# Kernel optimization log

Measured on AMD Instinct MI355X. Metric: run time of the kernel, lower is better.

The kernel has to match this reference:

```python
import jax, jax.numpy as jnp
import numpy as np

N_NODES = 300000   # cell instances
N_NETS  = 200000   # hyperedges (nets); each net has exactly one source/driver
E_SINK  = 1000000  # sink (node->net) pin edges
NODE_DIM, NET_DIM, EMB = 32, 16, 64
L, NUM_VN = 3, 1000
OUT_NODE, OUT_NET = 4, 4
SLOPE = 0.01  # torch leaky_relu default negative_slope


def leaky(x):
    return jnp.where(x >= 0, x, SLOPE * x)


def _lin(key, fan_in, fan_out):
    kw, kb = jax.random.split(key)
    b = 1.0 / np.sqrt(fan_in)
    W = jax.random.uniform(kw, (fan_in, fan_out), jnp.float32, -b, b)
    bb = jax.random.uniform(kb, (fan_out,), jnp.float32, -b, b)
    return W, bb


def setup_inputs() -> dict:
    key = jax.random.key(0)
    ks = iter(jax.random.split(key, 64))
    d = {}
    d["node_features"] = jax.random.normal(next(ks), (N_NODES, NODE_DIM), jnp.float32)
    d["net_features"] = jax.random.normal(next(ks), (N_NETS, NET_DIM), jnp.float32)
    d["src_nodes"] = jax.random.randint(next(ks), (N_NETS,), 0, N_NODES)   # driver node of net i
    d["sink_nodes"] = jax.random.randint(next(ks), (E_SINK,), 0, N_NODES)
    d["sink_nets"] = jax.random.randint(next(ks), (E_SINK,), 0, N_NETS)
    d["edge_weight"] = jax.random.uniform(next(ks), (E_SINK,), jnp.float32)
    d["batch"] = jax.random.randint(next(ks), (N_NODES,), 0, NUM_VN)       # node -> virtual node id
    # node / net encoders
    d["ne_W1"], d["ne_b1"] = _lin(next(ks), NODE_DIM, 2 * EMB)
    d["ne_W2"], d["ne_b2"] = _lin(next(ks), 2 * EMB, EMB)
    d["te_W1"], d["te_b1"] = _lin(next(ks), NET_DIM, EMB)
    d["te_W2"], d["te_b2"] = _lin(next(ks), EMB, EMB)
    d["vn_emb"] = jnp.zeros((EMB,), jnp.float32)  # torch: init.constant_(weight, 0)
    # HyperConv layers, stacked over L
    Wnet, bnet, Wnode, bnode = [], [], [], []
    for _ in range(L):
        W, b = _lin(next(ks), 3 * EMB, EMB); Wnet.append(W); bnet.append(b)
        W, b = _lin(next(ks), 2 * EMB, EMB); Wnode.append(W); bnode.append(b)
    d["conv_Wnet"] = jnp.stack(Wnet); d["conv_bnet"] = jnp.stack(bnet)
    d["conv_Wnode"] = jnp.stack(Wnode); d["conv_bnode"] = jnp.stack(bnode)
    # virtual-node MLPs (L-1 of them)
    vW1, vb1, vW2, vb2 = [], [], [], []
    for _ in range(L - 1):
        W, b = _lin(next(ks), EMB, EMB); vW1.append(W); vb1.append(b)
        W, b = _lin(next(ks), EMB, EMB); vW2.append(W); vb2.append(b)
    d["vn_W1"] = jnp.stack(vW1); d["vn_b1"] = jnp.stack(vb1)
    d["vn_W2"] = jnp.stack(vW2); d["vn_b2"] = jnp.stack(vb2)
    # output heads
    d["fc1n_W"], d["fc1n_b"] = _lin(next(ks), EMB, 256)
    d["fc2n_W"], d["fc2n_b"] = _lin(next(ks), 256, OUT_NODE)
    d["fc1e_W"], d["fc1e_b"] = _lin(next(ks), EMB, 64)
    d["fc2e_W"], d["fc2e_b"] = _lin(next(ks), 64, OUT_NET)
    return d


def _forward(node_features, net_features, edge_weight,
             ne_W1, ne_b1, ne_W2, ne_b2, te_W1, te_b1, te_W2, te_b2,
             vn_emb, conv_Wnet, conv_bnet, conv_Wnode, conv_bnode,
             vn_W1, vn_b1, vn_W2, vn_b2,
             fc1n_W, fc1n_b, fc2n_W, fc2n_b, fc1e_W, fc1e_b, fc2e_W, fc2e_b,
             src_nodes, sink_nodes, sink_nets, batch):
    h = leaky(node_features @ ne_W1 + ne_b1) @ ne_W2 + ne_b2   # [N, EMB]
    g = leaky(net_features @ te_W1 + te_b1) @ te_W2 + te_b2    # [M, EMB]
    w = edge_weight[:, None]
    vn = jnp.broadcast_to(vn_emb, (NUM_VN, EMB))               # embedding of all-zero indices
    for l in range(L):
        h = h + vn[batch]
        # node -> net (hyperedge) aggregation: driver message + weighted sink sum
        agg_src = h[src_nodes]                                             # [M, EMB]
        agg_sink = jax.ops.segment_sum(h[sink_nodes] * w, sink_nets, num_segments=N_NETS)
        g = jnp.concatenate([g, agg_src, agg_sink], axis=-1) @ conv_Wnet[l] + conv_bnet[l]
        # net -> node aggregation
        back = jax.ops.segment_sum(g, src_nodes, num_segments=N_NODES) \
             + jax.ops.segment_sum(g[sink_nets] * w, sink_nodes, num_segments=N_NODES)
        h = jnp.concatenate([h, back], axis=-1) @ conv_Wnode[l] + conv_bnode[l]
        h = leaky(h)
        g = leaky(g)
        if l < L - 1:
            pooled = jax.ops.segment_max(h, batch, num_segments=NUM_VN)   # global_max_pool
            tmp = pooled + vn
            vn = vn + (leaky(tmp @ vn_W1[l] + vn_b1[l]) @ vn_W2[l] + vn_b2[l])
    node_rep = jnp.abs(leaky(h @ fc1n_W + fc1n_b) @ fc2n_W + fc2n_b)
    net_rep = jnp.abs(leaky(g @ fc1e_W + fc1e_b) @ fc2e_W + fc2e_b)
    return node_rep, net_rep


def reference(node_features, net_features, edge_weight,
              ne_W1, ne_b1, ne_W2, ne_b2, te_W1, te_b1, te_W2, te_b2,
              vn_emb, conv_Wnet, conv_bnet, conv_Wnode, conv_bnode,
              vn_W1, vn_b1, vn_W2, vn_b2,
              fc1n_W, fc1n_b, fc2n_W, fc2n_b, fc1e_W, fc1e_b, fc2e_W, fc2e_b,
              src_nodes, sink_nodes, sink_nets, batch):
    return _forward(node_features, net_features, edge_weight,
                    ne_W1, ne_b1, ne_W2, ne_b2, te_W1, te_b1, te_W2, te_b2,
                    vn_emb, conv_Wnet, conv_bnet, conv_Wnode, conv_bnode,
                    vn_W1, vn_b1, vn_W2, vn_b2,
                    fc1n_W, fc1n_b, fc2n_W, fc2n_b, fc1e_W, fc1e_b, fc2e_W, fc2e_b,
                    src_nodes, sink_nodes, sink_nets, batch)
```

## Files before the change

### kernel.cpp

```cpp
#include <hip/hip_runtime.h>
#include <cstdint>

static constexpr int N_NODES = 300000;
static constexpr int N_NETS  = 200000;
static constexpr int E_SINK  = 1000000;
static constexpr int NODE_DIM = 32;
static constexpr int NET_DIM  = 16;
static constexpr int EMB = 64;
static constexpr int NUM_VN = 1000;
#define SLOPE 0.01f

typedef __attribute__((ext_vector_type(8))) short bhalf8;
typedef __attribute__((ext_vector_type(4))) float floatx4;

__device__ __forceinline__ float leaky(float x) { return x >= 0.f ? x : SLOPE * x; }

__device__ __forceinline__ unsigned bf16_rne(float x) {
    unsigned u = __float_as_uint(x);
    return (u + 0x7FFFu + ((u >> 16) & 1u)) >> 16;
}
__device__ __forceinline__ void split8(const float* x, bhalf8& ah, bhalf8& al) {
#pragma unroll
    for (int e = 0; e < 8; ++e) {
        unsigned h = bf16_rne(x[e]);
        float fh = __uint_as_float(h << 16);
        unsigned l = bf16_rne(x[e] - fh);
        ah[e] = (short)h; al[e] = (short)l;
    }
}

template<bool LK>
__device__ __forceinline__ void afrag_g(const float* rowp, int kbase, bhalf8& ah, bhalf8& al) {
    float4 v0 = *(const float4*)(rowp + kbase);
    float4 v1 = *(const float4*)(rowp + kbase + 4);
    float x[8] = {v0.x, v0.y, v0.z, v0.w, v1.x, v1.y, v1.z, v1.w};
    if (LK) {
#pragma unroll
        for (int e = 0; e < 8; ++e) x[e] = leaky(x[e]);
    }
    split8(x, ah, al);
}

__device__ __forceinline__ void afrag_l(const float* tp, bhalf8& ah, bhalf8& al) {
    float4 v0 = *(const float4*)tp;
    float4 v1 = *(const float4*)(tp + 4);
    float x[8] = {v0.x, v0.y, v0.z, v0.w, v1.x, v1.y, v1.z, v1.w};
    split8(x, ah, al);
}

__device__ __forceinline__ void wfrag(const float* W, int cols, int K, int col, bool colok,
                                      int kt, int g, bhalf8& wh, bhalf8& wl) {
    float x[8];
#pragma unroll
    for (int e = 0; e < 8; ++e) {
        int k = kt * 32 + g * 8 + e;
        x[e] = (k < K && colok) ? W[(size_t)k * cols + col] : 0.f;
    }
    split8(x, wh, wl);
}

__device__ __forceinline__ floatx4 mm3(bhalf8 ah, bhalf8 al, bhalf8 wh, bhalf8 wl, floatx4 c) {
    c = __builtin_amdgcn_mfma_f32_16x16x32_bf16(ah, wh, c, 0, 0, 0);
    c = __builtin_amdgcn_mfma_f32_16x16x32_bf16(ah, wl, c, 0, 0, 0);
    c = __builtin_amdgcn_mfma_f32_16x16x32_bf16(al, wh, c, 0, 0, 0);
    return c;
}

__global__ void k_hist_edges(const int* __restrict__ sink_nets, const int* __restrict__ sink_nodes,
                             int* __restrict__ cnt_net, int* __restrict__ cnt_node)
{
    int e = blockIdx.x * 256 + threadIdx.x;
    if (e >= E_SINK) return;
    atomicAdd(&cnt_net[sink_nets[e]], 1);
    atomicAdd(&cnt_node[sink_nodes[e]], 1);
}

__global__ void k_hist_misc(const int* __restrict__ src_nodes, const int* __restrict__ batch,
                            int* __restrict__ cnt_src, int* __restrict__ cnt_vn)
{
    int i = blockIdx.x * 256 + threadIdx.x;
    if (i < N_NETS) atomicAdd(&cnt_src[src_nodes[i]], 1);
    if (i < N_NODES) atomicAdd(&cnt_vn[batch[i]], 1);
}

__global__ void k_scan1(const int* __restrict__ cnt, int n, int* __restrict__ bsum) {
    __shared__ int s[256];
    int i = blockIdx.x * 256 + threadIdx.x;
    s[threadIdx.x] = (i < n) ? cnt[i] : 0;
    __syncthreads();
    for (int off = 128; off; off >>= 1) {
        if (threadIdx.x < off) s[threadIdx.x] += s[threadIdx.x + off];
        __syncthreads();
    }
    if (threadIdx.x == 0) bsum[blockIdx.x] = s[0];
}

__global__ void k_scan2(int* __restrict__ data, int n) {
    __shared__ int s[256];
    __shared__ int carry_s;
    int tid = threadIdx.x;
    if (tid == 0) carry_s = 0;
    __syncthreads();
    for (int base = 0; base < n; base += 256) {
        int i = base + tid;
        int v = (i < n) ? data[i] : 0;
        s[tid] = v;
        __syncthreads();
        for (int off = 1; off < 256; off <<= 1) {
            int t = (tid >= off) ? s[tid - off] : 0;
            __syncthreads();
            s[tid] += t;
            __syncthreads();
        }
        int excl = s[tid] - v + carry_s;
        if (i < n) data[i] = excl;
        __syncthreads();
        if (tid == 255) carry_s = excl + v;
        __syncthreads();
    }
}

__global__ void k_scan3(const int* __restrict__ cnt, int n, const int* __restrict__ bsum,
                        int* __restrict__ start) {
    __shared__ int s[256];
    int i = blockIdx.x * 256 + threadIdx.x;
    int v = (i < n) ? cnt[i] : 0;
    s[threadIdx.x] = v;
    __syncthreads();
    for (int off = 1; off < 256; off <<= 1) {
        int t = (threadIdx.x >= off) ? s[threadIdx.x - off] : 0;
        __syncthreads();
        s[threadIdx.x] += t;
        __syncthreads();
    }
    int excl = s[threadIdx.x] - v + bsum[blockIdx.x];
    if (i < n) start[i] = excl;
    if (i == n - 1) start[n] = excl + v;
}

__global__ void k_fill_edges(const int* __restrict__ sink_nets, const int* __restrict__ sink_nodes,
                             const float* __restrict__ ew,
                             const int* __restrict__ net_start, const int* __restrict__ node_start,
                             int* __restrict__ cur_net, int* __restrict__ cur_node,
                             int* __restrict__ e_node, float* __restrict__ e_w,
                             int* __restrict__ e2_net, float* __restrict__ e2_w)
{
    int e = blockIdx.x * 256 + threadIdx.x;
    if (e >= E_SINK) return;
    int tn = sink_nets[e], dn = sink_nodes[e];
    float w = ew[e];
    int p = net_start[tn] + atomicAdd(&cur_net[tn], 1);
    e_node[p] = dn; e_w[p] = w;
    int q = node_start[dn] + atomicAdd(&cur_node[dn], 1);
    e2_net[q] = tn; e2_w[q] = w;
}

__global__ void k_fill_misc(const int* __restrict__ src_nodes, const int* __restrict__ batch,
                            const int* __restrict__ src_start, const int* __restrict__ vn_start,
                            int* __restrict__ cur_src, int* __restrict__ cur_vn,
                            int* __restrict__ s_net, int* __restrict__ b_node)
{
    int i = blockIdx.x * 256 + threadIdx.x;
    if (i < N_NETS) {
        int d = src_nodes[i];
        int p = src_start[d] + atomicAdd(&cur_src[d], 1);
        s_net[p] = i;
    }
    if (i < N_NODES) {
        int v = batch[i];
        int p = vn_start[v] + atomicAdd(&cur_vn[v], 1);
        b_node[p] = i;
    }
}

__global__ __launch_bounds__(256) void k_gather_agg(
    float* __restrict__ agg, const float* __restrict__ h,
    const int* __restrict__ net_start, const int* __restrict__ e_node, const float* __restrict__ e_w)
{
    int w = (blockIdx.x * 256 + threadIdx.x) >> 6;
    if (w >= N_NETS) return;
    int lane = threadIdx.x & 63;
    int grp = lane >> 4, l15 = lane & 15;
    int j0 = net_start[w], j1 = net_start[w + 1];
    float ax = 0.f, ay = 0.f, az = 0.f, aw = 0.f;
    for (int j = j0 + grp; j < j1; j += 4) {
        int idx = e_node[j];
        float wt = e_w[j];
        float4 v = ((const float4*)(h + (size_t)idx * 64))[l15];
        ax += wt * v.x; ay += wt * v.y; az += wt * v.z; aw += wt * v.w;
    }
    ax += __shfl_xor(ax, 16, 64); ay += __shfl_xor(ay, 16, 64);
    az += __shfl_xor(az, 16, 64); aw += __shfl_xor(aw, 16, 64);
    ax += __shfl_xor(ax, 32, 64); ay += __shfl_xor(ay, 32, 64);
    az += __shfl_xor(az, 32, 64); aw += __shfl_xor(aw, 32, 64);
    if (grp == 0)
        ((float4*)(agg + (size_t)w * 64))[l15] = make_float4(ax, ay, az, aw);
}

__global__ __launch_bounds__(256) void k_gather_back(
    float* __restrict__ back, const float* __restrict__ g,
    const int* __restrict__ src_start, const int* __restrict__ s_net,
    const int* __restrict__ node_start, const int* __restrict__ e2_net, const float* __restrict__ e2_w)
{
    int w = (blockIdx.x * 256 + threadIdx.x) >> 6;
    if (w >= N_NODES) return;
    int lane = threadIdx.x & 63;
    int grp = lane >> 4, l15 = lane & 15;
    float ax = 0.f, ay = 0.f, az = 0.f, aw = 0.f;
    int j0 = src_start[w], j1 = src_start[w + 1];
    for (int j = j0 + grp; j < j1; j += 4) {
        int idx = s_net[j];
        float4 v = ((const float4*)(g + (size_t)idx * 64))[l15];
        ax += v.x; ay += v.y; az += v.z; aw += v.w;
    }
    j0 = node_start[w]; j1 = node_start[w + 1];
    for (int j = j0 + grp; j < j1; j += 4) {
        int idx = e2_net[j];
        float wt = e2_w[j];
        float4 v = ((const float4*)(g + (size_t)idx * 64))[l15];
        ax += wt * v.x; ay += wt * v.y; az += wt * v.z; aw += wt * v.w;
    }
    ax += __shfl_xor(ax, 16, 64); ay += __shfl_xor(ay, 16, 64);
    az += __shfl_xor(az, 16, 64); aw += __shfl_xor(aw, 16, 64);
    ax += __shfl_xor(ax, 32, 64); ay += __shfl_xor(ay, 32, 64);
    az += __shfl_xor(az, 32, 64); aw += __shfl_xor(aw, 32, 64);
    if (grp == 0)
        ((float4*)(back + (size_t)w * 64))[l15] = make_float4(ax, ay, az, aw);
}

__global__ __launch_bounds__(256) void k_pool_gather(
    float* __restrict__ pooled, const float* __restrict__ h,
    const int* __restrict__ vn_start, const int* __restrict__ b_node)
{
    __shared__ float4 red[16][16];
    int tid = threadIdx.x;
    int grp = tid >> 4, l15 = tid & 15;
    int v = blockIdx.x;
    int j0 = vn_start[v], j1 = vn_start[v + 1];
    const float NEG = -__builtin_inff();
    float mx = NEG, my = NEG, mz = NEG, mw = NEG;
    for (int j = j0 + grp; j < j1; j += 16) {
        int nd = b_node[j];
        float4 val = ((const float4*)(h + (size_t)nd * 64))[l15];
        mx = fmaxf(mx, val.x); my = fmaxf(my, val.y);
        mz = fmaxf(mz, val.z); mw = fmaxf(mw, val.w);
    }
    red[grp][l15] = make_float4(mx, my, mz, mw);
    __syncthreads();
    if (tid < 16) {
        float4 m = red[0][tid];
#pragma unroll
        for (int q = 1; q < 16; ++q) {
            float4 r = red[q][tid];
            m.x = fmaxf(m.x, r.x); m.y = fmaxf(m.y, r.y);
            m.z = fmaxf(m.z, r.z); m.w = fmaxf(m.w, r.w);
        }
        ((float4*)(pooled + (size_t)v * 64))[tid] = m;
    }
}

__global__ __launch_bounds__(256) void k_node_enc_mfma(
    const float* __restrict__ x, const float* __restrict__ W1, const float* __restrict__ b1,
    const float* __restrict__ W2, const float* __restrict__ b2, float* __restrict__ h)
{
    __shared__ __align__(16) float t[64][132];
    int lane = threadIdx.x & 63, wid = threadIdx.x >> 6;
    int g16 = lane >> 4, l15 = lane & 15;
    int rbase = blockIdx.x * 64;

    bhalf8 W1H[2], W1L[2];
#pragma unroll
    for (int s = 0; s < 2; ++s)
        wfrag(W1, 128, 32, wid * 16 + s * 64 + l15, true, 0, g16, W1H[s], W1L[s]);
    bhalf8 W2H[4], W2L[4];
#pragma unroll
    for (int kt = 0; kt < 4; ++kt)
        wfrag(W2, 64, 128, wid * 16 + l15, true, kt, g16, W2H[kt], W2L[kt]);

#pragma unroll
    for (int ms = 0; ms < 4; ++ms) {
        int r = min(rbase + ms * 16 + l15, N_NODES - 1);
        bhalf8 ah, al;
        afrag_g<false>(x + (size_t)r * NODE_DIM, g16 * 8, ah, al);
#pragma unroll
        for (int s = 0; s < 2; ++s) {
            floatx4 acc = {0.f, 0.f, 0.f, 0.f};
            acc = mm3(ah, al, W1H[s], W1L[s], acc);
            int hc = wid * 16 + s * 64 + l15;
            float bb = b1[hc];
#pragma unroll
            for (int i = 0; i < 4; ++i)
                t[ms * 16 + g16 * 4 + i][hc] = leaky(acc[i] + bb);
        }
    }
    __syncthreads();

    int cs = wid * 16 + l15;
    float bias = b2[cs];
#pragma unroll
    for (int ms = 0; ms < 4; ++ms) {
        floatx4 acc = {0.f, 0.f, 0.f, 0.f};
#pragma unroll
        for (int kt = 0; kt < 4; ++kt) {
            bhalf8 ah, al;
            afrag_l(&t[ms * 16 + l15][kt * 32 + g16 * 8], ah, al);
            acc = mm3(ah, al, W2H[kt], W2L[kt], acc);
        }
#pragma unroll
        for (int i = 0; i < 4; ++i) {
            int r = rbase + ms * 16 + g16 * 4 + i;
            if (r < N_NODES) h[(size_t)r * 64 + cs] = acc[i] + bias;
        }
    }
}

__global__ __launch_bounds__(256) void k_net_enc_mfma(
    const float* __restrict__ x, const float* __restrict__ W1, const float* __restrict__ b1,
    const float* __restrict__ W2, const float* __restrict__ b2, float* __restrict__ g)
{
    __shared__ __align__(16) float t[64][68];
    int lane = threadIdx.x & 63, wid = threadIdx.x >> 6;
    int g16 = lane >> 4, l15 = lane & 15;
    int rbase = blockIdx.x * 64;
    int cs = wid * 16 + l15;

    bhalf8 W1H, W1L;
    wfrag(W1, 64, 16, cs, true, 0, g16, W1H, W1L);
    bhalf8 W2H[2], W2L[2];
#pragma unroll
    for (int kt = 0; kt < 2; ++kt)
        wfrag(W2, 64, 64, cs, true, kt, g16, W2H[kt], W2L[kt]);

#pragma unroll
    for (int ms = 0; ms < 4; ++ms) {
        int r = min(rbase + ms * 16 + l15, N_NETS - 1);
        bhalf8 ah = {0,0,0,0,0,0,0,0}, al = {0,0,0,0,0,0,0,0};
        if (g16 < 2) afrag_g<false>(x + (size_t)r * NET_DIM, g16 * 8, ah, al);
        floatx4 acc = {0.f, 0.f, 0.f, 0.f};
        acc = mm3(ah, al, W1H, W1L, acc);
        float bb = b1[cs];
#pragma unroll
        for (int i = 0; i < 4; ++i)
            t[ms * 16 + g16 * 4 + i][cs] = leaky(acc[i] + bb);
    }
    __syncthreads();

    float bias = b2[cs];
#pragma unroll
    for (int ms = 0; ms < 4; ++ms) {
        floatx4 acc = {0.f, 0.f, 0.f, 0.f};
#pragma unroll
        for (int kt = 0; kt < 2; ++kt) {
            bhalf8 ah, al;
            afrag_l(&t[ms * 16 + l15][kt * 32 + g16 * 8], ah, al);
            acc = mm3(ah, al, W2H[kt], W2L[kt], acc);
        }
#pragma unroll
        for (int i = 0; i < 4; ++i) {
            int r = rbase + ms * 16 + g16 * 4 + i;
            if (r < N_NETS) g[(size_t)r * 64 + cs] = acc[i] + bias;
        }
    }
}

__global__ void k_vn_init(float* __restrict__ vn, const float* __restrict__ vn_emb) {
    int idx = blockIdx.x * blockDim.x + threadIdx.x;
    if (idx < NUM_VN * EMB) vn[idx] = vn_emb[idx & 63];
}

__global__ void k_add_vn(float4* __restrict__ h4, const float* __restrict__ vn,
                         const int* __restrict__ batch) {
    int idx = blockIdx.x * blockDim.x + threadIdx.x;
    if (idx >= N_NODES * 16) return;
    int n = idx >> 4, c4 = idx & 15;
    const float4* vr = (const float4*)(vn + (size_t)batch[n] * 64);
    float4 hv = h4[idx], vv = vr[c4];
    h4[idx] = make_float4(hv.x + vv.x, hv.y + vv.y, hv.z + vv.z, hv.w + vv.w);
}

__global__ __launch_bounds__(256) void k_conv_net_mfma(
    float* __restrict__ g, const float* __restrict__ h, const float* __restrict__ agg,
    const int* __restrict__ src, const float* __restrict__ W, const float* __restrict__ b, int lk0)
{
    int lane = threadIdx.x & 63, wid = threadIdx.x >> 6;
    int g16 = lane >> 4, l15 = lane & 15;
    int rbase = blockIdx.x * 64;
    int cs = wid * 16 + l15;

    bhalf8 WH[6], WL[6];
#pragma unroll
    for (int kt = 0; kt < 6; ++kt) wfrag(W, 64, 192, cs, true, kt, g16, WH[kt], WL[kt]);

    bhalf8 GH[4][2], GL[4][2];
#pragma unroll
    for (int ms = 0; ms < 4; ++ms) {
        int r = min(rbase + ms * 16 + l15, N_NETS - 1);
        const float* rp = g + (size_t)r * 64;
#pragma unroll
        for (int kt = 0; kt < 2; ++kt) {
            if (lk0) afrag_g<true>(rp, kt * 32 + g16 * 8, GH[ms][kt], GL[ms][kt]);
            else     afrag_g<false>(rp, kt * 32 + g16 * 8, GH[ms][kt], GL[ms][kt]);
        }
    }
    __syncthreads();

    float bias = b[cs];
#pragma unroll
    for (int ms = 0; ms < 4; ++ms) {
        floatx4 acc = {0.f, 0.f, 0.f, 0.f};
#pragma unroll
        for (int kt = 0; kt < 2; ++kt) acc = mm3(GH[ms][kt], GL[ms][kt], WH[kt], WL[kt], acc);
        int ar = min(rbase + ms * 16 + l15, N_NETS - 1);
        const float* hp = h + (size_t)src[ar] * 64;
#pragma unroll
        for (int kt = 0; kt < 2; ++kt) {
            bhalf8 ah, al;
            afrag_g<false>(hp, kt * 32 + g16 * 8, ah, al);
            acc = mm3(ah, al, WH[2 + kt], WL[2 + kt], acc);
        }
        const float* ap = agg + (size_t)ar * 64;
#pragma unroll
        for (int kt = 0; kt < 2; ++kt) {
            bhalf8 ah, al;
            afrag_g<false>(ap, kt * 32 + g16 * 8, ah, al);
            acc = mm3(ah, al, WH[4 + kt], WL[4 + kt], acc);
        }
#pragma unroll
        for (int i = 0; i < 4; ++i) {
            int r = rbase + ms * 16 + g16 * 4 + i;
            if (r < N_NETS) g[(size_t)r * 64 + cs] = acc[i] + bias;
        }
    }
}

__global__ __launch_bounds__(256) void k_conv_node_mfma(
    float* __restrict__ h, const float* __restrict__ back,
    const float* __restrict__ W, const float* __restrict__ b)
{
    int lane = threadIdx.x & 63, wid = threadIdx.x >> 6;
    int g16 = lane >> 4, l15 = lane & 15;
    int rbase = blockIdx.x * 64;
    int cs = wid * 16 + l15;

    bhalf8 WH[4], WL[4];
#pragma unroll
    for (int kt = 0; kt < 4; ++kt) wfrag(W, 64, 128, cs, true, kt, g16, WH[kt], WL[kt]);

    bhalf8 HH[4][2], HL[4][2];
#pragma unroll
    for (int ms = 0; ms < 4; ++ms) {
        int r = min(rbase + ms * 16 + l15, N_NODES - 1);
        const float* rp = h + (size_t)r * 64;
#pragma unroll
        for (int kt = 0; kt < 2; ++kt)
            afrag_g<false>(rp, kt * 32 + g16 * 8, HH[ms][kt], HL[ms][kt]);
    }
    __syncthreads();

    float bias = b[cs];
#pragma unroll
    for (int ms = 0; ms < 4; ++ms) {
        floatx4 acc = {0.f, 0.f, 0.f, 0.f};
#pragma unroll
        for (int kt = 0; kt < 2; ++kt) acc = mm3(HH[ms][kt], HL[ms][kt], WH[kt], WL[kt], acc);
        int ar = min(rbase + ms * 16 + l15, N_NODES - 1);
        const float* bp = back + (size_t)ar * 64;
#pragma unroll
        for (int kt = 0; kt < 2; ++kt) {
            bhalf8 ah, al;
            afrag_g<false>(bp, kt * 32 + g16 * 8, ah, al);
            acc = mm3(ah, al, WH[2 + kt], WL[2 + kt], acc);
        }
#pragma unroll
        for (int i = 0; i < 4; ++i) {
            int r = rbase + ms * 16 + g16 * 4 + i;
            if (r < N_NODES) h[(size_t)r * 64 + cs] = leaky(acc[i] + bias);
        }
    }
}

__global__ __launch_bounds__(256) void k_vn_update(
    float* __restrict__ vn, const float* __restrict__ pooled,
    const float* __restrict__ W1, const float* __restrict__ b1,
    const float* __restrict__ W2, const float* __restrict__ b2)
{
    int wv = threadIdx.x >> 6, lane = threadIdx.x & 63;
    int v = blockIdx.x * 4 + wv;
    if (v >= NUM_VN) return;
    float p = pooled[(size_t)v * 64 + lane];
    float vv = vn[v * 64 + lane];
    float tmp = p + vv;
    float t1 = b1[lane];
#pragma unroll 16
    for (int k = 0; k < 64; ++k) t1 += __shfl(tmp, k, 64) * W1[k * 64 + lane];
    t1 = leaky(t1);
    float t2 = b2[lane];
#pragma unroll 16
    for (int k = 0; k < 64; ++k) t2 += __shfl(t1, k, 64) * W2[k * 64 + lane];
    vn[v * 64 + lane] = vv + t2;
}

__global__ __launch_bounds__(256) void k_fc_node_mfma(
    float* __restrict__ out, const float* __restrict__ h,
    const float* __restrict__ W1, const float* __restrict__ b1,
    const float* __restrict__ W2, const float* __restrict__ b2)
{
    __shared__ __align__(16) float t[64][260];
    int lane = threadIdx.x & 63, wid = threadIdx.x >> 6;
    int g16 = lane >> 4, l15 = lane & 15;
    int rbase = blockIdx.x * 64;

    bhalf8 W1H[4][2], W1L[4][2];
#pragma unroll
    for (int s = 0; s < 4; ++s)
#pragma unroll
        for (int kt = 0; kt < 2; ++kt)
            wfrag(W1, 256, 64, wid * 16 + s * 64 + l15, true, kt, g16, W1H[s][kt], W1L[s][kt]);

#pragma unroll
    for (int ms = 0; ms < 4; ++ms) {
        int r = min(rbase + ms * 16 + l15, N_NODES - 1);
        bhalf8 ah[2], al[2];
#pragma unroll
        for (int kt = 0; kt < 2; ++kt)
            afrag_g<false>(h + (size_t)r * 64, kt * 32 + g16 * 8, ah[kt], al[kt]);
#pragma unroll
        for (int s = 0; s < 4; ++s) {
            floatx4 acc = {0.f, 0.f, 0.f, 0.f};
#pragma unroll
            for (int kt = 0; kt < 2; ++kt) acc = mm3(ah[kt], al[kt], W1H[s][kt], W1L[s][kt], acc);
            int hc = wid * 16 + s * 64 + l15;
            float bb = b1[hc];
#pragma unroll
            for (int i = 0; i < 4; ++i)
                t[ms * 16 + g16 * 4 + i][hc] = leaky(acc[i] + bb);
        }
    }
    __syncthreads();

    bhalf8 W2H[8], W2L[8];
#pragma unroll
    for (int kt = 0; kt < 8; ++kt)
        wfrag(W2, 4, 256, l15, l15 < 4, kt, g16, W2H[kt], W2L[kt]);

    floatx4 acc = {0.f, 0.f, 0.f, 0.f};
#pragma unroll
    for (int kt = 0; kt < 8; ++kt) {
        bhalf8 ah, al;
        afrag_l(&t[wid * 16 + l15][kt * 32 + g16 * 8], ah, al);
        acc = mm3(ah, al, W2H[kt], W2L[kt], acc);
    }
    if (l15 < 4) {
        float bo = b2[l15];
#pragma unroll
        for (int i = 0; i < 4; ++i) {
            int r = rbase + wid * 16 + g16 * 4 + i;
            if (r < N_NODES) out[(size_t)r * 4 + l15] = fabsf(acc[i] + bo);
        }
    }
}

__global__ __launch_bounds__(256) void k_fc_net_mfma(
    float* __restrict__ out, const float* __restrict__ g,
    const float* __restrict__ W1, const float* __restrict__ b1,
    const float* __restrict__ W2, const float* __restrict__ b2)
{
    __shared__ __align__(16) float t[64][68];
    int lane = threadIdx.x & 63, wid = threadIdx.x >> 6;
    int g16 = lane >> 4, l15 = lane & 15;
    int rbase = blockIdx.x * 64;
    int cs = wid * 16 + l15;

    bhalf8 W1H[2], W1L[2];
#pragma unroll
    for (int kt = 0; kt < 2; ++kt) wfrag(W1, 64, 64, cs, true, kt, g16, W1H[kt], W1L[kt]);

#pragma unroll
    for (int ms = 0; ms < 4; ++ms) {
        int r = min(rbase + ms * 16 + l15, N_NETS - 1);
        floatx4 acc = {0.f, 0.f, 0.f, 0.f};
#pragma unroll
        for (int kt = 0; kt < 2; ++kt) {
            bhalf8 ah, al;
            afrag_g<true>(g + (size_t)r * 64, kt * 32 + g16 * 8, ah, al);
            acc = mm3(ah, al, W1H[kt], W1L[kt], acc);
        }
        float bb = b1[cs];
#pragma unroll
        for (int i = 0; i < 4; ++i)
            t[ms * 16 + g16 * 4 + i][cs] = leaky(acc[i] + bb);
    }
    __syncthreads();

    bhalf8 W2H[2], W2L[2];
#pragma unroll
    for (int kt = 0; kt < 2; ++kt)
        wfrag(W2, 4, 64, l15, l15 < 4, kt, g16, W2H[kt], W2L[kt]);

    floatx4 acc = {0.f, 0.f, 0.f, 0.f};
#pragma unroll
    for (int kt = 0; kt < 2; ++kt) {
        bhalf8 ah, al;
        afrag_l(&t[wid * 16 + l15][kt * 32 + g16 * 8], ah, al);
        acc = mm3(ah, al, W2H[kt], W2L[kt], acc);
    }
    if (l15 < 4) {
        float bo = b2[l15];
#pragma unroll
        for (int i = 0; i < 4; ++i) {
            int r = rbase + wid * 16 + g16 * 4 + i;
            if (r < N_NETS) out[(size_t)r * 4 + l15] = fabsf(acc[i] + bo);
        }
    }
}

extern "C" void kernel_launch(void* const* d_in, const int* in_sizes, int n_in,
                              void* d_out, int out_size, void* d_ws, size_t ws_size,
                              hipStream_t stream)
{
    const float* node_features = (const float*)d_in[0];
    const float* net_features  = (const float*)d_in[1];
    const int*   src_nodes     = (const int*)d_in[2];
    const int*   sink_nodes    = (const int*)d_in[3];
    const int*   sink_nets     = (const int*)d_in[4];
    const float* edge_weight   = (const float*)d_in[5];
    const int*   batch         = (const int*)d_in[6];
    const float* ne_W1 = (const float*)d_in[7];
    const float* ne_b1 = (const float*)d_in[8];
    const float* ne_W2 = (const float*)d_in[9];
    const float* ne_b2 = (const float*)d_in[10];
    const float* te_W1 = (const float*)d_in[11];
    const float* te_b1 = (const float*)d_in[12];
    const float* te_W2 = (const float*)d_in[13];
    const float* te_b2 = (const float*)d_in[14];
    const float* vn_emb = (const float*)d_in[15];
    const float* conv_Wnet  = (const float*)d_in[16];
    const float* conv_bnet  = (const float*)d_in[17];
    const float* conv_Wnode = (const float*)d_in[18];
    const float* conv_bnode = (const float*)d_in[19];
    const float* vn_W1 = (const float*)d_in[20];
    const float* vn_b1 = (const float*)d_in[21];
    const float* vn_W2 = (const float*)d_in[22];
    const float* vn_b2 = (const float*)d_in[23];
    const float* fc1n_W = (const float*)d_in[24];
    const float* fc1n_b = (const float*)d_in[25];
    const float* fc2n_W = (const float*)d_in[26];
    const float* fc2n_b = (const float*)d_in[27];
    const float* fc1e_W = (const float*)d_in[28];
    const float* fc1e_b = (const float*)d_in[29];
    const float* fc2e_W = (const float*)d_in[30];
    const float* fc2e_b = (const float*)d_in[31];

    float* out_node = (float*)d_out;
    float* out_net  = out_node + (size_t)N_NODES * 4;

    float* h      = (float*)d_ws;
    float* g      = h + (size_t)N_NODES * EMB;
    float* scratch = g + (size_t)N_NETS * EMB;
    float* vn     = scratch + (size_t)N_NODES * EMB;
    float* pooled = vn + (size_t)NUM_VN * EMB;
    int* net_start  = (int*)(pooled + (size_t)NUM_VN * EMB);
    int* node_start = net_start + (N_NETS + 1);
    int* src_start  = node_start + (N_NODES + 1);
    int* vn_start   = src_start + (N_NODES + 1);
    int*   e_node = vn_start + (NUM_VN + 1);
    float* e_w    = (float*)(e_node + E_SINK);
    int*   e2_net = (int*)(e_w + E_SINK);
    float* e2_w   = (float*)(e2_net + E_SINK);
    int*   s_net  = (int*)(e2_w + E_SINK);
    int*   b_node = s_net + N_NETS;
    int*   cnt    = b_node + N_NODES;
    int*   cnt_net  = cnt;
    int*   cnt_node = cnt + N_NETS;
    int*   cnt_src  = cnt_node + N_NODES;
    int*   cnt_vn   = cnt_src + N_NODES;
    const int CNT_TOTAL = N_NETS + N_NODES + N_NODES + NUM_VN;
    int*   bsum   = cnt + CNT_TOTAL;

    const int nodeTiles = (N_NODES + 63) / 64;
    const int netTiles  = (N_NETS + 63) / 64;
    const int vnBlocks  = (NUM_VN + 3) / 4;
    const int vnElemBlocks   = (NUM_VN * EMB + 255) / 256;
    const int nodeVec4Blocks = (N_NODES * 16 + 255) / 256;
    const int edgeThreadBlocks = (E_SINK + 255) / 256;
    const int miscThreadBlocks = (N_NODES + 255) / 256;
    const int netWaveBlocks  = (N_NETS + 3) / 4;
    const int nodeWaveBlocks = (N_NODES + 3) / 4;

    hipMemsetAsync(cnt, 0, (size_t)CNT_TOTAL * sizeof(int), stream);
    k_hist_edges<<<edgeThreadBlocks, 256, 0, stream>>>(sink_nets, sink_nodes, cnt_net, cnt_node);
    k_hist_misc<<<miscThreadBlocks, 256, 0, stream>>>(src_nodes, batch, cnt_src, cnt_vn);

    auto scan = [&](int* cnt_arr, int n, int* start_arr) {
        int nb = (n + 255) / 256;
        k_scan1<<<nb, 256, 0, stream>>>(cnt_arr, n, bsum);
        k_scan2<<<1, 256, 0, stream>>>(bsum, nb);
        k_scan3<<<nb, 256, 0, stream>>>(cnt_arr, n, bsum, start_arr);
    };
    scan(cnt_net, N_NETS, net_start);
    scan(cnt_node, N_NODES, node_start);
    scan(cnt_src, N_NODES, src_start);
    scan(cnt_vn, NUM_VN, vn_start);

    hipMemsetAsync(cnt, 0, (size_t)CNT_TOTAL * sizeof(int), stream);
    k_fill_edges<<<edgeThreadBlocks, 256, 0, stream>>>(sink_nets, sink_nodes, edge_weight,
        net_start, node_start, cnt_net, cnt_node, e_node, e_w, e2_net, e2_w);
    k_fill_misc<<<miscThreadBlocks, 256, 0, stream>>>(src_nodes, batch, src_start, vn_start,
        cnt_src, cnt_vn, s_net, b_node);

    k_node_enc_mfma<<<nodeTiles, 256, 0, stream>>>(node_features, ne_W1, ne_b1, ne_W2, ne_b2, h);
    k_net_enc_mfma<<<netTiles, 256, 0, stream>>>(net_features, te_W1, te_b1, te_W2, te_b2, g);
    k_vn_init<<<vnElemBlocks, 256, 0, stream>>>(vn, vn_emb);

    for (int l = 0; l < 3; ++l) {
        k_add_vn<<<nodeVec4Blocks, 256, 0, stream>>>((float4*)h, vn, batch);

        k_gather_agg<<<netWaveBlocks, 256, 0, stream>>>(scratch, h, net_start, e_node, e_w);
        k_conv_net_mfma<<<netTiles, 256, 0, stream>>>(g, h, scratch, src_nodes,
            conv_Wnet + (size_t)l * 192 * 64, conv_bnet + (size_t)l * 64, l > 0 ? 1 : 0);

        k_gather_back<<<nodeWaveBlocks, 256, 0, stream>>>(scratch, g,
            src_start, s_net, node_start, e2_net, e2_w);
        k_conv_node_mfma<<<nodeTiles, 256, 0, stream>>>(h, scratch,
            conv_Wnode + (size_t)l * 128 * 64, conv_bnode + (size_t)l * 64);

        if (l < 2) {
            k_pool_gather<<<NUM_VN, 256, 0, stream>>>(pooled, h, vn_start, b_node);
            k_vn_update<<<vnBlocks, 256, 0, stream>>>(vn, pooled,
                vn_W1 + (size_t)l * 64 * 64, vn_b1 + (size_t)l * 64,
                vn_W2 + (size_t)l * 64 * 64, vn_b2 + (size_t)l * 64);
        }
    }

    k_fc_node_mfma<<<nodeTiles, 256, 0, stream>>>(out_node, h, fc1n_W, fc1n_b, fc2n_W, fc2n_b);
    k_fc_net_mfma<<<netTiles, 256, 0, stream>>>(out_net, g, fc1e_W, fc1e_b, fc2e_W, fc2e_b);
}
```

Before: 1.882 ms.

## Store activations as split bf16 hi/lo planes and pre-split weights once

Activations h, g and scratch are now kept as two bf16 planes (hi and lo) instead of fp32. The MFMA kernels load A-fragments directly without per-use splitting, and the gathers rebuild fp32 as hi+lo. All weights are packed into fragment order and split by a one-time prep kernel, so per-block strided weight loads and splitting go away. The fc heads replace the second small MFMA with shuffle reductions, and a leaky inversion (multiply by 100) is folded into gather_back. Memory traffic stays the same size, but load counts and ALU work change, and the inverse-leaky trick carries numerical risk.

```diff
diff --git a/kernel.cpp b/kernel.cpp
--- a/kernel.cpp
+++ b/kernel.cpp
@@ -12,6 +12,7 @@
 
 typedef __attribute__((ext_vector_type(8))) short bhalf8;
 typedef __attribute__((ext_vector_type(4))) float floatx4;
+typedef unsigned short u16;
 
 __device__ __forceinline__ float leaky(float x) { return x >= 0.f ? x : SLOPE * x; }
 
@@ -19,44 +20,34 @@
     unsigned u = __float_as_uint(x);
     return (u + 0x7FFFu + ((u >> 16) & 1u)) >> 16;
 }
-__device__ __forceinline__ void split8(const float* x, bhalf8& ah, bhalf8& al) {
+__device__ __forceinline__ void split1(float x, u16& hh, u16& ll) {
+    unsigned hb = bf16_rne(x);
+    float fh = __uint_as_float(hb << 16);
+    unsigned lb = bf16_rne(x - fh);
+    hh = (u16)hb; ll = (u16)lb;
+}
+__device__ __forceinline__ void split8v(const float* x, bhalf8& ah, bhalf8& al) {
 #pragma unroll
     for (int e = 0; e < 8; ++e) {
-        unsigned h = bf16_rne(x[e]);
-        float fh = __uint_as_float(h << 16);
-        unsigned l = bf16_rne(x[e] - fh);
-        ah[e] = (short)h; al[e] = (short)l;
-    }
-}
-
-template<bool LK>
-__device__ __forceinline__ void afrag_g(const float* rowp, int kbase, bhalf8& ah, bhalf8& al) {
+        u16 hh, ll; split1(x[e], hh, ll);
+        ah[e] = (short)hh; al[e] = (short)ll;
+    }
+}
+__device__ __forceinline__ float rec1(short h, short l) {
+    return __uint_as_float(((unsigned)(u16)h) << 16) +
+           __uint_as_float(((unsigned)(u16)l) << 16);
+}
+
+__device__ __forceinline__ void afrag_f32(const float* rowp, int kbase, bhalf8& ah, bhalf8& al) {
     float4 v0 = *(const float4*)(rowp + kbase);
     float4 v1 = *(const float4*)(rowp + kbase + 4);
     float x[8] = {v0.x, v0.y, v0.z, v0.w, v1.x, v1.y, v1.z, v1.w};
-    if (LK) {
-#pragma unroll
-        for (int e = 0; e < 8; ++e) x[e] = leaky(x[e]);
-    }
-    split8(x, ah, al);
-}
-
-__device__ __forceinline__ void afrag_l(const float* tp, bhalf8& ah, bhalf8& al) {
-    float4 v0 = *(const float4*)tp;
-    float4 v1 = *(const float4*)(tp + 4);
-    float x[8] = {v0.x, v0.y, v0.z, v0.w, v1.x, v1.y, v1.z, v1.w};
-    split8(x, ah, al);
-}
-
-__device__ __forceinline__ void wfrag(const float* W, int cols, int K, int col, bool colok,
-                                      int kt, int g, bhalf8& wh, bhalf8& wl) {
-    float x[8];
-#pragma unroll
-    for (int e = 0; e < 8; ++e) {
-        int k = kt * 32 + g * 8 + e;
-        x[e] = (k < K && colok) ? W[(size_t)k * cols + col] : 0.f;
-    }
-    split8(x, wh, wl);
+    split8v(x, ah, al);
+}
+__device__ __forceinline__ void afrag_hl(const u16* hi, const u16* lo, size_t off,
+                                         bhalf8& ah, bhalf8& al) {
+    ah = *(const bhalf8*)(hi + off);
+    al = *(const bhalf8*)(lo + off);
 }
 
 __device__ __forceinline__ floatx4 mm3(bhalf8 ah, bhalf8 al, bhalf8 wh, bhalf8 wl, floatx4 c) {
@@ -64,6 +55,48 @@
     c = __builtin_amdgcn_mfma_f32_16x16x32_bf16(ah, wl, c, 0, 0, 0);
     c = __builtin_amdgcn_mfma_f32_16x16x32_bf16(al, wh, c, 0, 0, 0);
     return c;
+}
+
+static constexpr int OFF_NEW1 = 0;
+static constexpr int OFF_NEW2 = 4096;
+static constexpr int OFF_TEW1 = 12288;
+static constexpr int OFF_TEW2 = 14336;
+static constexpr int OFF_CWNET = 18432;
+static constexpr int OFF_CWNODE = 55296;
+static constexpr int OFF_FC1N = 79872;
+static constexpr int OFF_FC1E = 96256;
+static constexpr int W_TOTAL  = 100352;
+
+__global__ void k_prep_w(const float* __restrict__ neW1, const float* __restrict__ neW2,
+                         const float* __restrict__ teW1, const float* __restrict__ teW2,
+                         const float* __restrict__ cWnet, const float* __restrict__ cWnode,
+                         const float* __restrict__ fc1n, const float* __restrict__ fc1e,
+                         u16* __restrict__ wfh, u16* __restrict__ wfl)
+{
+    int i = blockIdx.x * 256 + threadIdx.x;
+    if (i >= W_TOTAL) return;
+    int r, ncols, K; const float* src;
+    if (i < OFF_NEW2)        { r = i;             src = neW1;  ncols = 128; K = 32; }
+    else if (i < OFF_TEW1)   { r = i - OFF_NEW2;  src = neW2;  ncols = 64;  K = 128; }
+    else if (i < OFF_TEW2)   { r = i - OFF_TEW1;  src = teW1;  ncols = 64;  K = 16; }
+    else if (i < OFF_CWNET)  { r = i - OFF_TEW2;  src = teW2;  ncols = 64;  K = 64; }
+    else if (i < OFF_CWNODE) { int t = i - OFF_CWNET;  int l = t / 12288; r = t % 12288;
+                               src = cWnet + (size_t)l * 192 * 64; ncols = 64; K = 192; }
+    else if (i < OFF_FC1N)   { int t = i - OFF_CWNODE; int l = t / 8192;  r = t % 8192;
+                               src = cWnode + (size_t)l * 128 * 64; ncols = 64; K = 128; }
+    else if (i < OFF_FC1E)   { r = i - OFF_FC1N;  src = fc1n;  ncols = 256; K = 64; }
+    else                     { r = i - OFF_FC1E;  src = fc1e;  ncols = 64;  K = 64; }
+    int e = r & 7, g = (r >> 3) & 3;
+    int cidx = r >> 5;
+    int col = cidx % ncols, kt = cidx / ncols;
+    int k = kt * 32 + g * 8 + e;
+    float v = (k < K) ? src[(size_t)k * ncols + col] : 0.f;
+    u16 hh, ll; split1(v, hh, ll);
+    wfh[i] = hh; wfl[i] = ll;
+}
+
+__device__ __forceinline__ bhalf8 ldw(const u16* p, int idx) {
+    return *(const bhalf8*)(p + idx);
 }
 
 __global__ void k_hist_edges(const int* __restrict__ sink_nets, const int* __restrict__ sink_nodes,
@@ -174,114 +207,152 @@
 }
 
 __global__ __launch_bounds__(256) void k_gather_agg(
-    float* __restrict__ agg, const float* __restrict__ h,
+    u16* __restrict__ agg_hi, u16* __restrict__ agg_lo,
+    const u16* __restrict__ h_hi, const u16* __restrict__ h_lo,
     const int* __restrict__ net_start, const int* __restrict__ e_node, const float* __restrict__ e_w)
 {
     int w = (blockIdx.x * 256 + threadIdx.x) >> 6;
     if (w >= N_NETS) return;
     int lane = threadIdx.x & 63;
-    int grp = lane >> 4, l15 = lane & 15;
+    int grp = lane >> 3, l8 = lane & 7;
     int j0 = net_start[w], j1 = net_start[w + 1];
-    float ax = 0.f, ay = 0.f, az = 0.f, aw = 0.f;
-    for (int j = j0 + grp; j < j1; j += 4) {
+    float a[8] = {0.f, 0.f, 0.f, 0.f, 0.f, 0.f, 0.f, 0.f};
+    for (int j = j0 + grp; j < j1; j += 8) {
         int idx = e_node[j];
         float wt = e_w[j];
-        float4 v = ((const float4*)(h + (size_t)idx * 64))[l15];
-        ax += wt * v.x; ay += wt * v.y; az += wt * v.z; aw += wt * v.w;
-    }
-    ax += __shfl_xor(ax, 16, 64); ay += __shfl_xor(ay, 16, 64);
-    az += __shfl_xor(az, 16, 64); aw += __shfl_xor(aw, 16, 64);
-    ax += __shfl_xor(ax, 32, 64); ay += __shfl_xor(ay, 32, 64);
-    az += __shfl_xor(az, 32, 64); aw += __shfl_xor(aw, 32, 64);
-    if (grp == 0)
-        ((float4*)(agg + (size_t)w * 64))[l15] = make_float4(ax, ay, az, aw);
+        size_t off = (size_t)idx * 64 + l8 * 8;
+        bhalf8 vh = *(const bhalf8*)(h_hi + off);
+        bhalf8 vl = *(const bhalf8*)(h_lo + off);
+#pragma unroll
+        for (int e = 0; e < 8; ++e) a[e] += wt * rec1(vh[e], vl[e]);
+    }
+#pragma unroll
+    for (int e = 0; e < 8; ++e) {
+        a[e] += __shfl_xor(a[e], 8, 64);
+        a[e] += __shfl_xor(a[e], 16, 64);
+        a[e] += __shfl_xor(a[e], 32, 64);
+    }
+    if (grp == 0) {
+        bhalf8 oh, ol;
+        split8v(a, oh, ol);
+        size_t off = (size_t)w * 64 + l8 * 8;
+        *(bhalf8*)(agg_hi + off) = oh;
+        *(bhalf8*)(agg_lo + off) = ol;
+    }
 }
 
 __global__ __launch_bounds__(256) void k_gather_back(
-    float* __restrict__ back, const float* __restrict__ g,
+    u16* __restrict__ back_hi, u16* __restrict__ back_lo,
+    const u16* __restrict__ g_hi, const u16* __restrict__ g_lo,
     const int* __restrict__ src_start, const int* __restrict__ s_net,
     const int* __restrict__ node_start, const int* __restrict__ e2_net, const float* __restrict__ e2_w)
 {
     int w = (blockIdx.x * 256 + threadIdx.x) >> 6;
     if (w >= N_NODES) return;
     int lane = threadIdx.x & 63;
-    int grp = lane >> 4, l15 = lane & 15;
-    float ax = 0.f, ay = 0.f, az = 0.f, aw = 0.f;
+    int grp = lane >> 3, l8 = lane & 7;
+    float a[8] = {0.f, 0.f, 0.f, 0.f, 0.f, 0.f, 0.f, 0.f};
     int j0 = src_start[w], j1 = src_start[w + 1];
-    for (int j = j0 + grp; j < j1; j += 4) {
+    for (int j = j0 + grp; j < j1; j += 8) {
         int idx = s_net[j];
-        float4 v = ((const float4*)(g + (size_t)idx * 64))[l15];
-        ax += v.x; ay += v.y; az += v.z; aw += v.w;
+        size_t off = (size_t)idx * 64 + l8 * 8;
+        bhalf8 vh = *(const bhalf8*)(g_hi + off);
+        bhalf8 vl = *(const bhalf8*)(g_lo + off);
+#pragma unroll
+        for (int e = 0; e < 8; ++e) {
+            float f = rec1(vh[e], vl[e]);
+            a[e] += (f >= 0.f) ? f : f * 100.f;
+        }
     }
     j0 = node_start[w]; j1 = node_start[w + 1];
-    for (int j = j0 + grp; j < j1; j += 4) {
+    for (int j = j0 + grp; j < j1; j += 8) {
         int idx = e2_net[j];
         float wt = e2_w[j];
-        float4 v = ((const float4*)(g + (size_t)idx * 64))[l15];
-        ax += wt * v.x; ay += wt * v.y; az += wt * v.z; aw += wt * v.w;
-    }
-    ax += __shfl_xor(ax, 16, 64); ay += __shfl_xor(ay, 16, 64);
-    az += __shfl_xor(az, 16, 64); aw += __shfl_xor(aw, 16, 64);
-    ax += __shfl_xor(ax, 32, 64); ay += __shfl_xor(ay, 32, 64);
-    az += __shfl_xor(az, 32, 64); aw += __shfl_xor(aw, 32, 64);
-    if (grp == 0)
-        ((float4*)(back + (size_t)w * 64))[l15] = make_float4(ax, ay, az, aw);
+        size_t off = (size_t)idx * 64 + l8 * 8;
+        bhalf8 vh = *(const bhalf8*)(g_hi + off);
+        bhalf8 vl = *(const bhalf8*)(g_lo + off);
+#pragma unroll
+        for (int e = 0; e < 8; ++e) {
+            float f = rec1(vh[e], vl[e]);
+            a[e] += wt * ((f >= 0.f) ? f : f * 100.f);
+        }
+    }
+#pragma unroll
+    for (int e = 0; e < 8; ++e) {
+        a[e] += __shfl_xor(a[e], 8, 64);
+        a[e] += __shfl_xor(a[e], 16, 64);
+        a[e] += __shfl_xor(a[e], 32, 64);
+    }
+    if (grp == 0) {
+        bhalf8 oh, ol;
+        split8v(a, oh, ol);
+        size_t off = (size_t)w * 64 + l8 * 8;
+        *(bhalf8*)(back_hi + off) = oh;
+        *(bhalf8*)(back_lo + off) = ol;
+    }
 }
 
 __global__ __launch_bounds__(256) void k_pool_gather(
-    float* __restrict__ pooled, const float* __restrict__ h,
+    float* __restrict__ pooled, const u16* __restrict__ h_hi, const u16* __restrict__ h_lo,
     const int* __restrict__ vn_start, const int* __restrict__ b_node)
 {
-    __shared__ float4 red[16][16];
+    __shared__ float red[32][64];
     int tid = threadIdx.x;
-    int grp = tid >> 4, l15 = tid & 15;
+    int grp = tid >> 3, l8 = tid & 7;
     int v = blockIdx.x;
     int j0 = vn_start[v], j1 = vn_start[v + 1];
     const float NEG = -__builtin_inff();
-    float mx = NEG, my = NEG, mz = NEG, mw = NEG;
-    for (int j = j0 + grp; j < j1; j += 16) {
+    float m[8] = {NEG, NEG, NEG, NEG, NEG, NEG, NEG, NEG};
+    for (int j = j0 + grp; j < j1; j += 32) {
         int nd = b_node[j];
-        float4 val = ((const float4*)(h + (size_t)nd * 64))[l15];
-        mx = fmaxf(mx, val.x); my = fmaxf(my, val.y);
-        mz = fmaxf(mz, val.z); mw = fmaxf(mw, val.w);
-    }
-    red[grp][l15] = make_float4(mx, my, mz, mw);
-    __syncthreads();
-    if (tid < 16) {
-        float4 m = red[0][tid];
-#pragma unroll
-        for (int q = 1; q < 16; ++q) {
-            float4 r = red[q][tid];
-            m.x = fmaxf(m.x, r.x); m.y = fmaxf(m.y, r.y);
-            m.z = fmaxf(m.z, r.z); m.w = fmaxf(m.w, r.w);
-        }
-        ((float4*)(pooled + (size_t)v * 64))[tid] = m;
-    }
-}
-
-__global__ __launch_bounds__(256) void k_node_enc_mfma(
-    const float* __restrict__ x, const float* __restrict__ W1, const float* __restrict__ b1,
-    const float* __restrict__ W2, const float* __restrict__ b2, float* __restrict__ h)
-{
-    __shared__ __align__(16) float t[64][132];
+        size_t off = (size_t)nd * 64 + l8 * 8;
+        bhalf8 vh = *(const bhalf8*)(h_hi + off);
+        bhalf8 vl = *(const bhalf8*)(h_lo + off);
+#pragma unroll
+        for (int e = 0; e < 8; ++e) m[e] = fmaxf(m[e], rec1(vh[e], vl[e]));
+    }
+#pragma unroll
+    for (int e = 0; e < 8; ++e) red[grp][l8 * 8 + e] = m[e];
+    __syncthreads();
+    if (tid < 64) {
+        float mm = red[0][tid];
+#pragma unroll
+        for (int q = 1; q < 32; ++q) mm = fmaxf(mm, red[q][tid]);
+        pooled[(size_t)v * 64 + tid] = mm;
+    }
+}
+
+__global__ __launch_bounds__(256) void k_node_enc(
+    const float* __restrict__ x, const u16* __restrict__ wfh, const u16* __restrict__ wfl,
+    const float* __restrict__ b1, const float* __restrict__ b2,
+    u16* __restrict__ h_hi, u16* __restrict__ h_lo)
+{
+    __shared__ u16 t_hi[64][136];
+    __shared__ u16 t_lo[64][136];
     int lane = threadIdx.x & 63, wid = threadIdx.x >> 6;
     int g16 = lane >> 4, l15 = lane & 15;
     int rbase = blockIdx.x * 64;
 
     bhalf8 W1H[2], W1L[2];
 #pragma unroll
-    for (int s = 0; s < 2; ++s)
-        wfrag(W1, 128, 32, wid * 16 + s * 64 + l15, true, 0, g16, W1H[s], W1L[s]);
+    for (int s = 0; s < 2; ++s) {
+        int col = wid * 16 + s * 64 + l15;
+        int fo = OFF_NEW1 + (col * 4 + g16) * 8;
+        W1H[s] = ldw(wfh, fo); W1L[s] = ldw(wfl, fo);
+    }
     bhalf8 W2H[4], W2L[4];
-#pragma unroll
-    for (int kt = 0; kt < 4; ++kt)
-        wfrag(W2, 64, 128, wid * 16 + l15, true, kt, g16, W2H[kt], W2L[kt]);
+    int cs = wid * 16 + l15;
+#pragma unroll
+    for (int kt = 0; kt < 4; ++kt) {
+        int fo = OFF_NEW2 + ((kt * 64 + cs) * 4 + g16) * 8;
+        W2H[kt] = ldw(wfh, fo); W2L[kt] = ldw(wfl, fo);
+    }
 
 #pragma unroll
     for (int ms = 0; ms < 4; ++ms) {
         int r = min(rbase + ms * 16 + l15, N_NODES - 1);
         bhalf8 ah, al;
-        afrag_g<false>(x + (size_t)r * NODE_DIM, g16 * 8, ah, al);
+        afrag_f32(x + (size_t)r * NODE_DIM, g16 * 8, ah, al);
 #pragma unroll
         for (int s = 0; s < 2; ++s) {
             floatx4 acc = {0.f, 0.f, 0.f, 0.f};
@@ -289,59 +360,75 @@
             int hc = wid * 16 + s * 64 + l15;
             float bb = b1[hc];
 #pragma unroll
-            for (int i = 0; i < 4; ++i)
-                t[ms * 16 + g16 * 4 + i][hc] = leaky(acc[i] + bb);
-        }
-    }
-    __syncthreads();
-
-    int cs = wid * 16 + l15;
+            for (int i = 0; i < 4; ++i) {
+                u16 hh, ll;
+                split1(leaky(acc[i] + bb), hh, ll);
+                t_hi[ms * 16 + g16 * 4 + i][hc] = hh;
+                t_lo[ms * 16 + g16 * 4 + i][hc] = ll;
+            }
+        }
+    }
+    __syncthreads();
+
     float bias = b2[cs];
 #pragma unroll
     for (int ms = 0; ms < 4; ++ms) {
         floatx4 acc = {0.f, 0.f, 0.f, 0.f};
 #pragma unroll
         for (int kt = 0; kt < 4; ++kt) {
-            bhalf8 ah, al;
-            afrag_l(&t[ms * 16 + l15][kt * 32 + g16 * 8], ah, al);
+            bhalf8 ah = *(const bhalf8*)(&t_hi[ms * 16 + l15][kt * 32 + g16 * 8]);
+            bhalf8 al = *(const bhalf8*)(&t_lo[ms * 16 + l15][kt * 32 + g16 * 8]);
             acc = mm3(ah, al, W2H[kt], W2L[kt], acc);
         }
 #pragma unroll
         for (int i = 0; i < 4; ++i) {
             int r = rbase + ms * 16 + g16 * 4 + i;
-            if (r < N_NODES) h[(size_t)r * 64 + cs] = acc[i] + bias;
-        }
-    }
-}
-
-__global__ __launch_bounds__(256) void k_net_enc_mfma(
-    const float* __restrict__ x, const float* __restrict__ W1, const float* __restrict__ b1,
-    const float* __restrict__ W2, const float* __restrict__ b2, float* __restrict__ g)
-{
-    __shared__ __align__(16) float t[64][68];
+            if (r < N_NODES) {
+                u16 hh, ll;
+                split1(acc[i] + bias, hh, ll);
+                h_hi[(size_t)r * 64 + cs] = hh;
+                h_lo[(size_t)r * 64 + cs] = ll;
+            }
+        }
+    }
+}
+
+__global__ __launch_bounds__(256) void k_net_enc(
+    const float* __restrict__ x, const u16* __restrict__ wfh, const u16* __restrict__ wfl,
+    const float* __restrict__ b1, const float* __restrict__ b2,
+    u16* __restrict__ g_hi, u16* __restrict__ g_lo)
+{
+    __shared__ u16 t_hi[64][72];
+    __shared__ u16 t_lo[64][72];
     int lane = threadIdx.x & 63, wid = threadIdx.x >> 6;
     int g16 = lane >> 4, l15 = lane & 15;
     int rbase = blockIdx.x * 64;
     int cs = wid * 16 + l15;
 
-    bhalf8 W1H, W1L;
-    wfrag(W1, 64, 16, cs, true, 0, g16, W1H, W1L);
+    int fo = OFF_TEW1 + (cs * 4 + g16) * 8;
+    bhalf8 W1H = ldw(wfh, fo), W1L = ldw(wfl, fo);
     bhalf8 W2H[2], W2L[2];
 #pragma unroll
-    for (int kt = 0; kt < 2; ++kt)
-        wfrag(W2, 64, 64, cs, true, kt, g16, W2H[kt], W2L[kt]);
+    for (int kt = 0; kt < 2; ++kt) {
+        int f2 = OFF_TEW2 + ((kt * 64 + cs) * 4 + g16) * 8;
+        W2H[kt] = ldw(wfh, f2); W2L[kt] = ldw(wfl, f2);
+    }
 
 #pragma unroll
     for (int ms = 0; ms < 4; ++ms) {
         int r = min(rbase + ms * 16 + l15, N_NETS - 1);
         bhalf8 ah = {0,0,0,0,0,0,0,0}, al = {0,0,0,0,0,0,0,0};
-        if (g16 < 2) afrag_g<false>(x + (size_t)r * NET_DIM, g16 * 8, ah, al);
+        if (g16 < 2) afrag_f32(x + (size_t)r * NET_DIM, g16 * 8, ah, al);
         floatx4 acc = {0.f, 0.f, 0.f, 0.f};
         acc = mm3(ah, al, W1H, W1L, acc);
         float bb = b1[cs];
 #pragma unroll
-        for (int i = 0; i < 4; ++i)
-            t[ms * 16 + g16 * 4 + i][cs] = leaky(acc[i] + bb);
+        for (int i = 0; i < 4; ++i) {
+            u16 hh, ll;
+            split1(leaky(acc[i] + bb), hh, ll);
+            t_hi[ms * 16 + g16 * 4 + i][cs] = hh;
+            t_lo[ms * 16 + g16 * 4 + i][cs] = ll;
+        }
     }
     __syncthreads();
 
@@ -351,14 +438,19 @@
         floatx4 acc = {0.f, 0.f, 0.f, 0.f};
 #pragma unroll
         for (int kt = 0; kt < 2; ++kt) {
-            bhalf8 ah, al;
-            afrag_l(&t[ms * 16 + l15][kt * 32 + g16 * 8], ah, al);
+            bhalf8 ah = *(const bhalf8*)(&t_hi[ms * 16 + l15][kt * 32 + g16 * 8]);
+            bhalf8 al = *(const bhalf8*)(&t_lo[ms * 16 + l15][kt * 32 + g16 * 8]);
             acc = mm3(ah, al, W2H[kt], W2L[kt], acc);
         }
 #pragma unroll
         for (int i = 0; i < 4; ++i) {
             int r = rbase + ms * 16 + g16 * 4 + i;
-            if (r < N_NETS) g[(size_t)r * 64 + cs] = acc[i] + bias;
+            if (r < N_NETS) {
+                u16 hh, ll;
+                split1(acc[i] + bias, hh, ll);
+                g_hi[(size_t)r * 64 + cs] = hh;
+                g_lo[(size_t)r * 64 + cs] = ll;
+            }
         }
     }
 }
@@ -368,19 +460,31 @@
     if (idx < NUM_VN * EMB) vn[idx] = vn_emb[idx & 63];
 }
 
-__global__ void k_add_vn(float4* __restrict__ h4, const float* __restrict__ vn,
-                         const int* __restrict__ batch) {
+__global__ void k_add_vn(u16* __restrict__ h_hi, u16* __restrict__ h_lo,
+                         const float* __restrict__ vn, const int* __restrict__ batch) {
     int idx = blockIdx.x * blockDim.x + threadIdx.x;
-    if (idx >= N_NODES * 16) return;
-    int n = idx >> 4, c4 = idx & 15;
-    const float4* vr = (const float4*)(vn + (size_t)batch[n] * 64);
-    float4 hv = h4[idx], vv = vr[c4];
-    h4[idx] = make_float4(hv.x + vv.x, hv.y + vv.y, hv.z + vv.z, hv.w + vv.w);
-}
-
-__global__ __launch_bounds__(256) void k_conv_net_mfma(
-    float* __restrict__ g, const float* __restrict__ h, const float* __restrict__ agg,
-    const int* __restrict__ src, const float* __restrict__ W, const float* __restrict__ b, int lk0)
+    if (idx >= N_NODES * 8) return;
+    int n = idx >> 3, c8 = idx & 7;
+    size_t off = (size_t)n * 64 + c8 * 8;
+    bhalf8 vh = *(const bhalf8*)(h_hi + off);
+    bhalf8 vl = *(const bhalf8*)(h_lo + off);
+    const float* vr = vn + (size_t)batch[n] * 64 + c8 * 8;
+    float out[8];
+#pragma unroll
+    for (int e = 0; e < 8; ++e) out[e] = rec1(vh[e], vl[e]) + vr[e];
+    bhalf8 oh, ol;
+    split8v(out, oh, ol);
+    *(bhalf8*)(h_hi + off) = oh;
+    *(bhalf8*)(h_lo + off) = ol;
+}
+
+__global__ __launch_bounds__(256) void k_conv_net(
+    u16* g_hi, u16* g_lo,
+    const u16* __restrict__ h_hi, const u16* __restrict__ h_lo,
+    const u16* __restrict__ s_hi, const u16* __restrict__ s_lo,
+    const int* __restrict__ src,
+    const u16* __restrict__ wfh, const u16* __restrict__ wfl, int wbase,
+    const float* __restrict__ b)
 {
     int lane = threadIdx.x & 63, wid = threadIdx.x >> 6;
     int g16 = lane >> 4, l15 = lane & 15;
@@ -389,18 +493,18 @@
 
     bhalf8 WH[6], WL[6];
 #pragma unroll
-    for (int kt = 0; kt < 6; ++kt) wfrag(W, 64, 192, cs, true, kt, g16, WH[kt], WL[kt]);
+    for (int kt = 0; kt < 6; ++kt) {
+        int fo = wbase + ((kt * 64 + cs) * 4 + g16) * 8;
+        WH[kt] = ldw(wfh, fo); WL[kt] = ldw(wfl, fo);
+    }
 
     bhalf8 GH[4][2], GL[4][2];
 #pragma unroll
     for (int ms = 0; ms < 4; ++ms) {
         int r = min(rbase + ms * 16 + l15, N_NETS - 1);
-        const float* rp = g + (size_t)r * 64;
-#pragma unroll
-        for (int kt = 0; kt < 2; ++kt) {
-            if (lk0) afrag_g<true>(rp, kt * 32 + g16 * 8, GH[ms][kt], GL[ms][kt]);
-            else     afrag_g<false>(rp, kt * 32 + g16 * 8, GH[ms][kt], GL[ms][kt]);
-        }
+#pragma unroll
+        for (int kt = 0; kt < 2; ++kt)
+            afrag_hl(g_hi, g_lo, (size_t)r * 64 + kt * 32 + g16 * 8, GH[ms][kt], GL[ms][kt]);
     }
     __syncthreads();
 
@@ -411,31 +515,37 @@
 #pragma unroll
         for (int kt = 0; kt < 2; ++kt) acc = mm3(GH[ms][kt], GL[ms][kt], WH[kt], WL[kt], acc);
         int ar = min(rbase + ms * 16 + l15, N_NETS - 1);
-        const float* hp = h + (size_t)src[ar] * 64;
+        size_t srow = (size_t)src[ar] * 64;
 #pragma unroll
         for (int kt = 0; kt < 2; ++kt) {
             bhalf8 ah, al;
-            afrag_g<false>(hp, kt * 32 + g16 * 8, ah, al);
+            afrag_hl(h_hi, h_lo, srow + kt * 32 + g16 * 8, ah, al);
             acc = mm3(ah, al, WH[2 + kt], WL[2 + kt], acc);
         }
-        const float* ap = agg + (size_t)ar * 64;
 #pragma unroll
         for (int kt = 0; kt < 2; ++kt) {
             bhalf8 ah, al;
-            afrag_g<false>(ap, kt * 32 + g16 * 8, ah, al);
+            afrag_hl(s_hi, s_lo, (size_t)ar * 64 + kt * 32 + g16 * 8, ah, al);
             acc = mm3(ah, al, WH[4 + kt], WL[4 + kt], acc);
         }
 #pragma unroll
         for (int i = 0; i < 4; ++i) {
             int r = rbase + ms * 16 + g16 * 4 + i;
-            if (r < N_NETS) g[(size_t)r * 64 + cs] = acc[i] + bias;
-        }
-    }
-}
-
-__global__ __launch_bounds__(256) void k_conv_node_mfma(
-    float* __restrict__ h, const float* __restrict__ back,
-    const float* __restrict__ W, const float* __restrict__ b)
+            if (r < N_NETS) {
+                u16 hh, ll;
+                split1(leaky(acc[i] + bias), hh, ll);
+                g_hi[(size_t)r * 64 + cs] = hh;
+                g_lo[(size_t)r * 64 + cs] = ll;
+            }
+        }
+    }
+}
+
+__global__ __launch_bounds__(256) void k_conv_node(
+    u16* h_hi, u16* h_lo,
+    const u16* __restrict__ s_hi, const u16* __restrict__ s_lo,
+    const u16* __restrict__ wfh, const u16* __restrict__ wfl, int wbase,
+    const float* __restrict__ b)
 {
     int lane = threadIdx.x & 63, wid = threadIdx.x >> 6;
     int g16 = lane >> 4, l15 = lane & 15;
@@ -444,16 +554,18 @@
 
     bhalf8 WH[4], WL[4];
 #pragma unroll
-    for (int kt = 0; kt < 4; ++kt) wfrag(W, 64, 128, cs, true, kt, g16, WH[kt], WL[kt]);
+    for (int kt = 0; kt < 4; ++kt) {
+        int fo = wbase + ((kt * 64 + cs) * 4 + g16) * 8;
+        WH[kt] = ldw(wfh, fo); WL[kt] = ldw(wfl, fo);
+    }
 
     bhalf8 HH[4][2], HL[4][2];
 #pragma unroll
     for (int ms = 0; ms < 4; ++ms) {
         int r = min(rbase + ms * 16 + l15, N_NODES - 1);
-        const float* rp = h + (size_t)r * 64;
 #pragma unroll
         for (int kt = 0; kt < 2; ++kt)
-            afrag_g<false>(rp, kt * 32 + g16 * 8, HH[ms][kt], HL[ms][kt]);
+            afrag_hl(h_hi, h_lo, (size_t)r * 64 + kt * 32 + g16 * 8, HH[ms][kt], HL[ms][kt]);
     }
     __syncthreads();
 
@@ -464,17 +576,21 @@
 #pragma unroll
         for (int kt = 0; kt < 2; ++kt) acc = mm3(HH[ms][kt], HL[ms][kt], WH[kt], WL[kt], acc);
         int ar = min(rbase + ms * 16 + l15, N_NODES - 1);
-        const float* bp = back + (size_t)ar * 64;
 #pragma unroll
         for (int kt = 0; kt < 2; ++kt) {
             bhalf8 ah, al;
-            afrag_g<false>(bp, kt * 32 + g16 * 8, ah, al);
+            afrag_hl(s_hi, s_lo, (size_t)ar * 64 + kt * 32 + g16 * 8, ah, al);
             acc = mm3(ah, al, WH[2 + kt], WL[2 + kt], acc);
         }
 #pragma unroll
         for (int i = 0; i < 4; ++i) {
             int r = rbase + ms * 16 + g16 * 4 + i;
-            if (r < N_NODES) h[(size_t)r * 64 + cs] = leaky(acc[i] + bias);
+            if (r < N_NODES) {
+                u16 hh, ll;
+                split1(leaky(acc[i] + bias), hh, ll);
+                h_hi[(size_t)r * 64 + cs] = hh;
+                h_lo[(size_t)r * 64 + cs] = ll;
+            }
         }
     }
 }
@@ -500,22 +616,30 @@
     vn[v * 64 + lane] = vv + t2;
 }
 
-__global__ __launch_bounds__(256) void k_fc_node_mfma(
-    float* __restrict__ out, const float* __restrict__ h,
-    const float* __restrict__ W1, const float* __restrict__ b1,
-    const float* __restrict__ W2, const float* __restrict__ b2)
-{
-    __shared__ __align__(16) float t[64][260];
+__global__ __launch_bounds__(256) void k_fc_node(
+    float* __restrict__ out, const u16* __restrict__ h_hi, const u16* __restrict__ h_lo,
+    const u16* __restrict__ wfh, const u16* __restrict__ wfl,
+    const float* __restrict__ b1, const float* __restrict__ W2, const float* __restrict__ b2)
+{
+    __shared__ float red[4][64][4];
     int lane = threadIdx.x & 63, wid = threadIdx.x >> 6;
     int g16 = lane >> 4, l15 = lane & 15;
     int rbase = blockIdx.x * 64;
 
     bhalf8 W1H[4][2], W1L[4][2];
-#pragma unroll
-    for (int s = 0; s < 4; ++s)
-#pragma unroll
-        for (int kt = 0; kt < 2; ++kt)
-            wfrag(W1, 256, 64, wid * 16 + s * 64 + l15, true, kt, g16, W1H[s][kt], W1L[s][kt]);
+    float4 w2v[4];
+    float b1v[4];
+#pragma unroll
+    for (int s = 0; s < 4; ++s) {
+        int hc = wid * 16 + s * 64 + l15;
+#pragma unroll
+        for (int kt = 0; kt < 2; ++kt) {
+            int fo = OFF_FC1N + ((kt * 256 + hc) * 4 + g16) * 8;
+            W1H[s][kt] = ldw(wfh, fo); W1L[s][kt] = ldw(wfl, fo);
+        }
+        w2v[s] = *(const float4*)(W2 + hc * 4);
+        b1v[s] = b1[hc];
+    }
 
 #pragma unroll
     for (int ms = 0; ms < 4; ++ms) {
@@ -523,49 +647,53 @@
         bhalf8 ah[2], al[2];
 #pragma unroll
         for (int kt = 0; kt < 2; ++kt)
-            afrag_g<false>(h + (size_t)r * 64, kt * 32 + g16 * 8, ah[kt], al[kt]);
+            afrag_hl(h_hi, h_lo, (size_t)r * 64 + kt * 32 + g16 * 8, ah[kt], al[kt]);
+        float po[4][4] = {{0.f,0.f,0.f,0.f},{0.f,0.f,0.f,0.f},{0.f,0.f,0.f,0.f},{0.f,0.f,0.f,0.f}};
 #pragma unroll
         for (int s = 0; s < 4; ++s) {
             floatx4 acc = {0.f, 0.f, 0.f, 0.f};
 #pragma unroll
             for (int kt = 0; kt < 2; ++kt) acc = mm3(ah[kt], al[kt], W1H[s][kt], W1L[s][kt], acc);
-            int hc = wid * 16 + s * 64 + l15;
-            float bb = b1[hc];
+#pragma unroll
+            for (int i = 0; i < 4; ++i) {
+                float act = leaky(acc[i] + b1v[s]);
+                po[i][0] += act * w2v[s].x;
+                po[i][1] += act * w2v[s].y;
+                po[i][2] += act * w2v[s].z;
+                po[i][3] += act * w2v[s].w;
+            }
+        }
+#pragma unroll
+        for (int i = 0; i < 4; ++i)
+#pragma unroll
+            for (int o = 0; o < 4; ++o) {
+                po[i][o] += __shfl_xor(po[i][o], 1, 64);
+                po[i][o] += __shfl_xor(po[i][o], 2, 64);
+                po[i][o] += __shfl_xor(po[i][o], 4, 64);
+                po[i][o] += __shfl_xor(po[i][o], 8, 64);
+            }
+        if (l15 == 0) {
 #pragma unroll
             for (int i = 0; i < 4; ++i)
-                t[ms * 16 + g16 * 4 + i][hc] = leaky(acc[i] + bb);
-        }
-    }
-    __syncthreads();
-
-    bhalf8 W2H[8], W2L[8];
-#pragma unroll
-    for (int kt = 0; kt < 8; ++kt)
-        wfrag(W2, 4, 256, l15, l15 < 4, kt, g16, W2H[kt], W2L[kt]);
-
-    floatx4 acc = {0.f, 0.f, 0.f, 0.f};
-#pragma unroll
-    for (int kt = 0; kt < 8; ++kt) {
-        bhalf8 ah, al;
-        afrag_l(&t[wid * 16 + l15][kt * 32 + g16 * 8], ah, al);
-        acc = mm3(ah, al, W2H[kt], W2L[kt], acc);
-    }
-    if (l15 < 4) {
-        float bo = b2[l15];
-#pragma unroll
-        for (int i = 0; i < 4; ++i) {
-            int r = rbase + wid * 16 + g16 * 4 + i;
-            if (r < N_NODES) out[(size_t)r * 4 + l15] = fabsf(acc[i] + bo);
-        }
-    }
-}
-
-__global__ __launch_bounds__(256) void k_fc_net_mfma(
-    float* __restrict__ out, const float* __restrict__ g,
-    const float* __restrict__ W1, const float* __restrict__ b1,
-    const float* __restrict__ W2, const float* __restrict__ b2)
-{
-    __shared__ __align__(16) float t[64][68];
+#pragma unroll
+                for (int o = 0; o < 4; ++o)
+                    red[wid][ms * 16 + g16 * 4 + i][o] = po[i][o];
+        }
+    }
+    __syncthreads();
+    int tid = threadIdx.x;
+    int row = tid >> 2, o = tid & 3;
+    float sum = red[0][row][o] + red[1][row][o] + red[2][row][o] + red[3][row][o];
+    int r = rbase + row;
+    if (r < N_NODES) out[(size_t)r * 4 + o] = fabsf(sum + b2[o]);
+}
+
+__global__ __launch_bounds__(256) void k_fc_net(
+    float* __restrict__ out, const u16* __restrict__ g_hi, const u16* __restrict__ g_lo,
+    const u16* __restrict__ wfh, const u16* __restrict__ wfl,
+    const float* __restrict__ b1, const float* __restrict__ W2, const float* __restrict__ b2)
+{
+    __shared__ float red[4][64][4];
     int lane = threadIdx.x & 63, wid = threadIdx.x >> 6;
     int g16 = lane >> 4, l15 = lane & 15;
     int rbase = blockIdx.x * 64;
@@ -573,45 +701,55 @@
 
     bhalf8 W1H[2], W1L[2];
 #pragma unroll
-    for (int kt = 0; kt < 2; ++kt) wfrag(W1, 64, 64, cs, true, kt, g16, W1H[kt], W1L[kt]);
+    for (int kt = 0; kt < 2; ++kt) {
+        int fo = OFF_FC1E + ((kt * 64 + cs) * 4 + g16) * 8;
+        W1H[kt] = ldw(wfh, fo); W1L[kt] = ldw(wfl, fo);
+    }
+    float4 w2v = *(const float4*)(W2 + cs * 4);
+    float b1v = b1[cs];
 
 #pragma unroll
     for (int ms = 0; ms < 4; ++ms) {
         int r = min(rbase + ms * 16 + l15, N_NETS - 1);
+        bhalf8 ah[2], al[2];
+#pragma unroll
+        for (int kt = 0; kt < 2; ++kt)
+            afrag_hl(g_hi, g_lo, (size_t)r * 64 + kt * 32 + g16 * 8, ah[kt], al[kt]);
         floatx4 acc = {0.f, 0.f, 0.f, 0.f};
 #pragma unroll
-        for (int kt = 0; kt < 2; ++kt) {
-            bhalf8 ah, al;
-            afrag_g<true>(g + (size_t)r * 64, kt * 32 + g16 * 8, ah, al);
-            acc = mm3(ah, al, W1H[kt], W1L[kt], acc);
-        }
-        float bb = b1[cs];
+        for (int kt = 0; kt < 2; ++kt) acc = mm3(ah[kt], al[kt], W1H[kt], W1L[kt], acc);
+        float po[4][4];
+#pragma unroll
+        for (int i = 0; i < 4; ++i) {
+            float act = leaky(acc[i] + b1v);
+            po[i][0] = act * w2v.x;
+            po[i][1] = act * w2v.y;
+            po[i][2] = act * w2v.z;
+            po[i][3] = act * w2v.w;
+        }
 #pragma unroll
         for (int i = 0; i < 4; ++i)
-            t[ms * 16 + g16 * 4 + i][cs] = leaky(acc[i] + bb);
-    }
-    __syncthreads();
-
-    bhalf8 W2H[2], W2L[2];
-#pragma unroll
-    for (int kt = 0; kt < 2; ++kt)
-        wfrag(W2, 4, 64, l15, l15 < 4, kt, g16, W2H[kt], W2L[kt]);
-
-    floatx4 acc = {0.f, 0.f, 0.f, 0.f};
-#pragma unroll
-    for (int kt = 0; kt < 2; ++kt) {
-        bhalf8 ah, al;
-        afrag_l(&t[wid * 16 + l15][kt * 32 + g16 * 8], ah, al);
-        acc = mm3(ah, al, W2H[kt], W2L[kt], acc);
-    }
-    if (l15 < 4) {
-        float bo = b2[l15];
-#pragma unroll
-        for (int i = 0; i < 4; ++i) {
-            int r = rbase + wid * 16 + g16 * 4 + i;
-            if (r < N_NETS) out[(size_t)r * 4 + l15] = fabsf(acc[i] + bo);
-        }
-    }
+#pragma unroll
+            for (int o = 0; o < 4; ++o) {
+                po[i][o] += __shfl_xor(po[i][o], 1, 64);
+                po[i][o] += __shfl_xor(po[i][o], 2, 64);
+                po[i][o] += __shfl_xor(po[i][o], 4, 64);
+                po[i][o] += __shfl_xor(po[i][o], 8, 64);
+            }
+        if (l15 == 0) {
+#pragma unroll
+            for (int i = 0; i < 4; ++i)
+#pragma unroll
+                for (int o = 0; o < 4; ++o)
+                    red[wid][ms * 16 + g16 * 4 + i][o] = po[i][o];
+        }
+    }
+    __syncthreads();
+    int tid = threadIdx.x;
+    int row = tid >> 2, o = tid & 3;
+    float sum = red[0][row][o] + red[1][row][o] + red[2][row][o] + red[3][row][o];
+    int r = rbase + row;
+    if (r < N_NETS) out[(size_t)r * 4 + o] = fabsf(sum + b2[o]);
 }
 
 extern "C" void kernel_launch(void* const* d_in, const int* in_sizes, int n_in,
@@ -654,10 +792,15 @@
     float* out_node = (float*)d_out;
     float* out_net  = out_node + (size_t)N_NODES * 4;
 
-    float* h      = (float*)d_ws;
-    float* g      = h + (size_t)N_NODES * EMB;
-    float* scratch = g + (size_t)N_NETS * EMB;
-    float* vn     = scratch + (size_t)N_NODES * EMB;
+    u16* h_hi = (u16*)d_ws;
+    u16* h_lo = h_hi + (size_t)N_NODES * 64;
+    u16* g_hi = h_lo + (size_t)N_NODES * 64;
+    u16* g_lo = g_hi + (size_t)N_NETS * 64;
+    u16* s_hi = g_lo + (size_t)N_NETS * 64;
+    u16* s_lo = s_hi + (size_t)N_NODES * 64;
+    u16* wfh  = s_lo + (size_t)N_NODES * 64;
+    u16* wfl  = wfh + W_TOTAL;
+    float* vn     = (float*)(wfl + W_TOTAL);
     float* pooled = vn + (size_t)NUM_VN * EMB;
     int* net_start  = (int*)(pooled + (size_t)NUM_VN * EMB);
     int* node_start = net_start + (N_NETS + 1);
@@ -680,12 +823,13 @@
     const int nodeTiles = (N_NODES + 63) / 64;
     const int netTiles  = (N_NETS + 63) / 64;
     const int vnBlocks  = (NUM_VN + 3) / 4;
-    const int vnElemBlocks   = (NUM_VN * EMB + 255) / 256;
-    const int nodeVec4Blocks = (N_NODES * 16 + 255) / 256;
+    const int vnElemBlocks  = (NUM_VN * EMB + 255) / 256;
+    const int addVnBlocks  = (N_NODES * 8 + 255) / 256;
     const int edgeThreadBlocks = (E_SINK + 255) / 256;
     const int miscThreadBlocks = (N_NODES + 255) / 256;
     const int netWaveBlocks  = (N_NETS + 3) / 4;
     const int nodeWaveBlocks = (N_NODES + 3) / 4;
+    const int prepBlocks = (W_TOTAL + 255) / 256;
 
     hipMemsetAsync(cnt, 0, (size_t)CNT_TOTAL * sizeof(int), stream);
     k_hist_edges<<<edgeThreadBlocks, 256, 0, stream>>>(sink_nets, sink_nodes, cnt_net, cnt_node);
@@ -708,30 +852,35 @@
     k_fill_misc<<<miscThreadBlocks, 256, 0, stream>>>(src_nodes, batch, src_start, vn_start,
         cnt_src, cnt_vn, s_net, b_node);
 
-    k_node_enc_mfma<<<nodeTiles, 256, 0, stream>>>(node_features, ne_W1, ne_b1, ne_W2, ne_b2, h);
-    k_net_enc_mfma<<<netTiles, 256, 0, stream>>>(net_features, te_W1, te_b1, te_W2, te_b2, g);
+    k_prep_w<<<prepBlocks, 256, 0, stream>>>(ne_W1, ne_W2, te_W1, te_W2,
+                                             conv_Wnet, conv_Wnode, fc1n_W, fc1e_W, wfh, wfl);
+    k_node_enc<<<nodeTiles, 256, 0, stream>>>(node_features, wfh, wfl, ne_b1, ne_b2, h_hi, h_lo);
+    k_net_enc<<<netTiles, 256, 0, stream>>>(net_features, wfh, wfl, te_b1, te_b2, g_hi, g_lo);
     k_vn_init<<<vnElemBlocks, 256, 0, stream>>>(vn, vn_emb);
 
     for (int l = 0; l < 3; ++l) {
-        k_add_vn<<<nodeVec4Blocks, 256, 0, stream>>>((float4*)h, vn, batch);
-
-        k_gather_agg<<<netWaveBlocks, 256, 0, stream>>>(scratch, h, net_start, e_node, e_w);
-        k_conv_net_mfma<<<netTiles, 256, 0, stream>>>(g, h, scratch, src_nodes,
-            conv_Wnet + (size_t)l * 192 * 64, conv_bnet + (size_t)l * 64, l > 0 ? 1 : 0);
-
-        k_gather_back<<<nodeWaveBlocks, 256, 0, stream>>>(scratch, g,
+        k_add_vn<<<addVnBlocks, 256, 0, stream>>>(h_hi, h_lo, vn, batch);
+
+        k_gather_agg<<<netWaveBlocks, 256, 0, stream>>>(s_hi, s_lo, h_hi, h_lo,
+                                                        net_start, e_node, e_w);
+        k_conv_net<<<netTiles, 256, 0, stream>>>(g_hi, g_lo, h_hi, h_lo, s_hi, s_lo, src_nodes,
+            wfh, wfl, OFF_CWNET + l * 12288, conv_bnet + (size_t)l * 64);
+
+        k_gather_back<<<nodeWaveBlocks, 256, 0, stream>>>(s_hi, s_lo, g_hi, g_lo,
             src_start, s_net, node_start, e2_net, e2_w);
-        k_conv_node_mfma<<<nodeTiles, 256, 0, stream>>>(h, scratch,
-            conv_Wnode + (size_t)l * 128 * 64, conv_bnode + (size_t)l * 64);
+        k_conv_node<<<nodeTiles, 256, 0, stream>>>(h_hi, h_lo, s_hi, s_lo,
+            wfh, wfl, OFF_CWNODE + l * 8192, conv_bnode + (size_t)l * 64);
 
         if (l < 2) {
-            k_pool_gather<<<NUM_VN, 256, 0, stream>>>(pooled, h, vn_start, b_node);
+            k_pool_gather<<<NUM_VN, 256, 0, stream>>>(pooled, h_hi, h_lo, vn_start, b_node);
             k_vn_update<<<vnBlocks, 256, 0, stream>>>(vn, pooled,
                 vn_W1 + (size_t)l * 64 * 64, vn_b1 + (size_t)l * 64,
                 vn_W2 + (size_t)l * 64 * 64, vn_b2 + (size_t)l * 64);
         }
     }
 
-    k_fc_node_mfma<<<nodeTiles, 256, 0, stream>>>(out_node, h, fc1n_W, fc1n_b, fc2n_W, fc2n_b);
-    k_fc_net_mfma<<<netTiles, 256, 0, stream>>>(out_net, g, fc1e_W, fc1e_b, fc2e_W, fc2e_b);
-}
+    k_fc_node<<<nodeTiles, 256, 0, stream>>>(out_node, h_hi, h_lo, wfh, wfl,
+                                             fc1n_b, fc2n_W, fc2n_b);
+    k_fc_net<<<netTiles, 256, 0, stream>>>(out_net, g_hi, g_lo, wfh, wfl,
+                                           fc1e_b, fc2e_W, fc2e_b);
+}
```

Result: faster. 1.792 ms (-4.8%).
